# Kernel optimization log

Measured on AMD Instinct MI355X. Metric: run time of the kernel, lower is better.

The kernel has to match this reference:

```python
import jax, jax.numpy as jnp
import numpy as np

WINDOW = 128
CAUSAL = True
LOOK_BACKWARD = 1
LOOK_FORWARD = 0  # causal forces look_forward = 0


def _look_around(x, backward, forward, pad_value, dim):
    # pad along window axis (axis=1), then concat shifted slices along `dim`
    nw = x.shape[1]
    pad_cfg = [(0, 0)] * x.ndim
    pad_cfg[1] = (backward, forward)
    padded = jnp.pad(x, pad_cfg, constant_values=pad_value)
    slices = [padded[:, i:i + nw] for i in range(forward + backward + 1)]
    return jnp.concatenate(slices, axis=dim)


def setup_inputs() -> dict:
    key = jax.random.key(0)
    kq, kk, kv = jax.random.split(key, 3)
    shape = (2, 16, 4096, 64)
    return {
        "q": jax.random.normal(kq, shape, dtype=jnp.float32),
        "k": jax.random.normal(kk, shape, dtype=jnp.float32),
        "v": jax.random.normal(kv, shape, dtype=jnp.float32),
    }


def reference(q, k, v):
    b, h, t, e = q.shape
    scale = e ** (-0.5)
    windows = t // WINDOW  # t assumed divisible by WINDOW (pad_to_multiple is no-op)

    # merge batch and heads, bucket into windows
    bq = q.reshape(b * h, windows, WINDOW, e)
    bk = k.reshape(b * h, windows, WINDOW, e)
    bv = v.reshape(b * h, windows, WINDOW, e)

    # look-around gather of key/value windows: j-dim = WINDOW*(1+back+fwd)
    bk = _look_around(bk, LOOK_BACKWARD, LOOK_FORWARD, 0.0, dim=2)
    bv = _look_around(bv, LOOK_BACKWARD, LOOK_FORWARD, 0.0, dim=2)

    # positional indices for masking
    bq_t = jnp.arange(t).reshape(1, windows, WINDOW)
    bq_k = _look_around(bq_t, LOOK_BACKWARD, LOOK_FORWARD, -1, dim=2)

    mask = (bq_k == -1)[:, :, None, :]  # (1, w, 1, j) padded positions
    if CAUSAL:
        mask = mask | (bq_t[:, :, :, None] < bq_k[:, :, None, :])

    dots = jnp.einsum('bwie,bwje->bwij', bq * scale, bk)
    mask_value = -jnp.finfo(dots.dtype).max
    dots = jnp.where(mask, mask_value, dots)
    attn = jax.nn.softmax(dots.astype(jnp.float32), axis=-1).astype(dots.dtype)
    out = jnp.einsum('bwij,bwje->bwie', attn, bv)
    return out.reshape(b, h, t, e)
```

## Files before the change

kernel.cpp:

```cpp
#include <hip/hip_runtime.h>

#define T_DIM 4096
#define E_DIM 64
#define WIN   128
#define NWIN  (T_DIM / WIN)
#define KS_LD 72
#define VT_LD 136
#define OS_LD 68

typedef __bf16  bf16x4 __attribute__((ext_vector_type(4)));
typedef __bf16  bf16x8 __attribute__((ext_vector_type(8)));
typedef float   f32x16 __attribute__((ext_vector_type(16)));

__global__ __launch_bounds__(256, 4)
void la_fwd(const float* __restrict__ Q, const float* __restrict__ K,
            const float* __restrict__ V, float* __restrict__ O)
{
  __shared__ __align__(16) unsigned char lds_raw[35840];
  __bf16* Ks = (__bf16*)(lds_raw);
  __bf16* Vt = (__bf16*)(lds_raw + 18432);
  float*  Os = (float*)(lds_raw);

  const int tid  = threadIdx.x;
  const int lane = tid & 63;
  const int wid  = tid >> 6;
  const int col  = lane & 31;
  const int half = lane >> 5;

  const int flat = blockIdx.x;
  const int w  = (flat >> 3) & 31;
  const int bh = (flat & 7) * 4 + (flat >> 8);

  const float* Qb = Q + (size_t)bh * T_DIM * E_DIM;
  const float* Kb = K + (size_t)bh * T_DIM * E_DIM;
  const float* Vb = V + (size_t)bh * T_DIM * E_DIM;
  float*       Ob = O + (size_t)bh * T_DIM * E_DIM;

  const int q0 = w * WIN;
  const int eg = tid & 15;
  const int j0 = (tid >> 4) * 8;

  const float* kp1 = Kb + (size_t)q0 * E_DIM;
  const float* vp1 = Vb + (size_t)q0 * E_DIM;
  const float* kp0 = kp1 - WIN * E_DIM;
  const float* vp0 = vp1 - WIN * E_DIM;

  auto stageK = [&](const float* kp) {
    float4 kf[8];
#pragma unroll
    for (int i = 0; i < 8; ++i) kf[i] = *(const float4*)(kp + (i << 10) + (tid << 2));
#pragma unroll
    for (int i = 0; i < 8; ++i) {
      const int fi = (i << 10) + (tid << 2);
      bf16x4 k4;
      k4[0]=(__bf16)kf[i].x; k4[1]=(__bf16)kf[i].y; k4[2]=(__bf16)kf[i].z; k4[3]=(__bf16)kf[i].w;
      *(bf16x4*)(&Ks[(fi >> 6) * KS_LD + (fi & 63)]) = k4;
    }
  };
  auto stageV = [&](const float* vp) {
    float4 vf[8];
#pragma unroll
    for (int r = 0; r < 8; ++r)
      vf[r] = *(const float4*)(vp + (size_t)(j0 + r) * E_DIM + eg * 4);
#pragma unroll
    for (int c = 0; c < 4; ++c) {
      bf16x8 t;
#pragma unroll
      for (int r = 0; r < 8; ++r) t[r] = (__bf16)(((const float*)&vf[r])[c]);
      *(bf16x8*)(&Vt[(eg * 4 + c) * VT_LD + j0]) = t;
    }
  };

  const float QS = 0.125f * 1.44269504088896340736f;
  float4 qf[8];
  {
    const float* qrow = Qb + (size_t)(q0 + wid * 32 + col) * E_DIM;
#pragma unroll
    for (int c = 0; c < 4; ++c) {
      qf[2 * c]     = *(const float4*)(qrow + c * 16 + half * 8);
      qf[2 * c + 1] = *(const float4*)(qrow + c * 16 + half * 8 + 4);
    }
  }
  if (w > 0) { stageK(kp0); stageV(vp0); }
  else       { stageK(kp1); stageV(vp1); }

  bf16x8 bq[4];
#pragma unroll
  for (int c = 0; c < 4; ++c) {
    const float* x = (const float*)&qf[2 * c];
    const float* y = (const float*)&qf[2 * c + 1];
    bf16x8 a;
    a[0]=(__bf16)(x[0]*QS); a[1]=(__bf16)(x[1]*QS); a[2]=(__bf16)(x[2]*QS); a[3]=(__bf16)(x[3]*QS);
    a[4]=(__bf16)(y[0]*QS); a[5]=(__bf16)(y[1]*QS); a[6]=(__bf16)(y[2]*QS); a[7]=(__bf16)(y[3]*QS);
    bq[c] = a;
  }

  float  lsum = 0.0f;
  f32x16 oacc[2];
#pragma unroll
  for (int et = 0; et < 2; ++et)
#pragma unroll
    for (int r = 0; r < 16; ++r) oacc[et][r] = 0.0f;

  __syncthreads();

  auto kb_step = [&](int kb, bool diag) {
    f32x16 s;
#pragma unroll
    for (int r = 0; r < 16; ++r) s[r] = 0.0f;
#pragma unroll
    for (int c = 0; c < 4; ++c) {
      const bf16x8 a = *(const bf16x8*)(&Ks[(kb * 32 + col) * KS_LD + c * 16 + half * 8]);
      s = __builtin_amdgcn_mfma_f32_32x32x16_bf16(a, bq[c], s, 0, 0, 0);
    }
    float pr[16];
#pragma unroll
    for (int r = 0; r < 16; ++r) {
      const int key = (r & 3) + 8 * (r >> 2) + 4 * half;
      float sv = s[r];
      if (diag && key > col) sv = -3.0e38f;
      const float p = __builtin_amdgcn_exp2f(sv);
      lsum += p;
      pr[r] = p;
    }
#pragma unroll
    for (int g = 0; g < 2; ++g) {
      int A0, A1, B0, B1;
      asm("v_cvt_pk_bf16_f32 %0, %1, %2" : "=v"(A0) : "v"(pr[8*g+0]), "v"(pr[8*g+1]));
      asm("v_cvt_pk_bf16_f32 %0, %1, %2" : "=v"(A1) : "v"(pr[8*g+2]), "v"(pr[8*g+3]));
      asm("v_cvt_pk_bf16_f32 %0, %1, %2" : "=v"(B0) : "v"(pr[8*g+4]), "v"(pr[8*g+5]));
      asm("v_cvt_pk_bf16_f32 %0, %1, %2" : "=v"(B1) : "v"(pr[8*g+6]), "v"(pr[8*g+7]));
      asm("v_permlane32_swap_b32 %0, %1" : "+v"(A0), "+v"(B0));
      asm("v_permlane32_swap_b32 %0, %1" : "+v"(A1), "+v"(B1));
      union { int d[4]; bf16x8 v; } u;
      u.d[0] = A0; u.d[1] = A1; u.d[2] = B0; u.d[3] = B1;
      const int j0v = kb * 32 + g * 16 + half * 8;
#pragma unroll
      for (int et = 0; et < 2; ++et) {
        const bf16x8 bv = *(const bf16x8*)(&Vt[(et * 32 + col) * VT_LD + j0v]);
        oacc[et] = __builtin_amdgcn_mfma_f32_32x32x16_bf16(u.v, bv, oacc[et], 0, 0, 0);
      }
    }
  };

  if (w > 0) {
#pragma unroll
    for (int kb = 0; kb < 4; ++kb) kb_step(kb, false);
    __syncthreads();
    stageK(kp1);
    stageV(vp1);
    __syncthreads();
  }
#pragma unroll
  for (int kb = 0; kb < 4; ++kb)
    if (kb <= wid) kb_step(kb, kb == wid);

  float xx = lsum, yy = lsum;
  asm("v_permlane32_swap_b32 %0, %1" : "+v"(xx), "+v"(yy));
  const float ltot = xx + yy;

  __syncthreads();
#pragma unroll
  for (int r = 0; r < 16; ++r) {
    const int row = (r & 3) + 8 * (r >> 2) + 4 * half;
    const float lq   = __int_as_float(__builtin_amdgcn_ds_bpermute(row << 2, __float_as_int(ltot)));
    const float rinv = __builtin_amdgcn_rcpf(lq);
    Os[(wid * 32 + row) * OS_LD + col]      = oacc[0][r] * rinv;
    Os[(wid * 32 + row) * OS_LD + col + 32] = oacc[1][r] * rinv;
  }
  __syncthreads();
  {
    float* ob = Ob + (size_t)q0 * E_DIM;
#pragma unroll
    for (int i = 0; i < 8; ++i) {
      const int fi = (i << 10) + (tid << 2);
      const float4 o4 = *(const float4*)(&Os[(fi >> 6) * OS_LD + (fi & 63)]);
      *(float4*)(ob + fi) = o4;
    }
  }
}

extern "C" void kernel_launch(void* const* d_in, const int* in_sizes, int n_in,
                              void* d_out, int out_size, void* d_ws, size_t ws_size,
                              hipStream_t stream) {
  const float* Q = (const float*)d_in[0];
  const float* K = (const float*)d_in[1];
  const float* V = (const float*)d_in[2];
  float*       O = (float*)d_out;
  const int bh = in_sizes[0] / (T_DIM * E_DIM);
  la_fwd<<<dim3(NWIN * bh), 256, 0, stream>>>(Q, K, V, O);
}
```

Measured before the change: 140.8 us.

## Prefetch current K/V window into registers and swizzle LDS layouts

Issues global loads for both the previous and current K/V windows up front, holding the current window converted to bf16 in registers so its latency overlaps the first window's compute. LDS padding is replaced with XOR swizzles for K and transposed V, which shrinks shared memory to 32KB. The block index mapping also changes from a custom flattened remap to a plain 2D grid. The trade-off is higher register pressure from holding the prefetched tiles, and the output staging buffer loses its padding, which may cause bank conflicts.

```diff
diff --git a/kernel.cpp b/kernel.cpp
--- a/kernel.cpp
+++ b/kernel.cpp
@@ -4,9 +4,8 @@
 #define E_DIM 64
 #define WIN   128
 #define NWIN  (T_DIM / WIN)
-#define KS_LD 72
-#define VT_LD 136
-#define OS_LD 68
+#define K_B   16384
+#define V_B   16384
 
 typedef __bf16  bf16x4 __attribute__((ext_vector_type(4)));
 typedef __bf16  bf16x8 __attribute__((ext_vector_type(8)));
@@ -16,10 +15,10 @@
 void la_fwd(const float* __restrict__ Q, const float* __restrict__ K,
             const float* __restrict__ V, float* __restrict__ O)
 {
-  __shared__ __align__(16) unsigned char lds_raw[35840];
-  __bf16* Ks = (__bf16*)(lds_raw);
-  __bf16* Vt = (__bf16*)(lds_raw + 18432);
-  float*  Os = (float*)(lds_raw);
+  __shared__ __align__(16) unsigned char lds_raw[K_B + V_B];
+  unsigned char* KsB = lds_raw;
+  unsigned char* VtB = lds_raw + K_B;
+  float*         Os  = (float*)lds_raw;
 
   const int tid  = threadIdx.x;
   const int lane = tid & 63;
@@ -27,72 +26,105 @@
   const int col  = lane & 31;
   const int half = lane >> 5;
 
-  const int flat = blockIdx.x;
-  const int w  = (flat >> 3) & 31;
-  const int bh = (flat & 7) * 4 + (flat >> 8);
+  const int w  = blockIdx.x;
+  const int bh = blockIdx.y;
 
   const float* Qb = Q + (size_t)bh * T_DIM * E_DIM;
   const float* Kb = K + (size_t)bh * T_DIM * E_DIM;
   const float* Vb = V + (size_t)bh * T_DIM * E_DIM;
   float*       Ob = O + (size_t)bh * T_DIM * E_DIM;
 
-  const int q0 = w * WIN;
-  const int eg = tid & 15;
-  const int j0 = (tid >> 4) * 8;
-
-  const float* kp1 = Kb + (size_t)q0 * E_DIM;
-  const float* vp1 = Vb + (size_t)q0 * E_DIM;
-  const float* kp0 = kp1 - WIN * E_DIM;
-  const float* vp0 = vp1 - WIN * E_DIM;
-
-  auto stageK = [&](const float* kp) {
-    float4 kf[8];
-#pragma unroll
-    for (int i = 0; i < 8; ++i) kf[i] = *(const float4*)(kp + (i << 10) + (tid << 2));
+  const int q0  = w * WIN;
+  const int eg  = tid & 15;
+  const int j0v = (tid >> 4) * 8;
+
+  auto ldK = [&](int kr0, float4* f) {
+    const float* p = Kb + (size_t)kr0 * E_DIM;
+#pragma unroll
+    for (int i = 0; i < 8; ++i) f[i] = *(const float4*)(p + (i << 10) + (tid << 2));
+  };
+  auto ldV = [&](int kr0, float4* f) {
+    const float* p = Vb + (size_t)kr0 * E_DIM;
+#pragma unroll
+    for (int r = 0; r < 8; ++r)
+      f[r] = *(const float4*)(p + (size_t)(j0v + r) * E_DIM + eg * 4);
+  };
+  auto cvtK = [&](const float4* f, bf16x4* b) {
 #pragma unroll
     for (int i = 0; i < 8; ++i) {
-      const int fi = (i << 10) + (tid << 2);
       bf16x4 k4;
-      k4[0]=(__bf16)kf[i].x; k4[1]=(__bf16)kf[i].y; k4[2]=(__bf16)kf[i].z; k4[3]=(__bf16)kf[i].w;
-      *(bf16x4*)(&Ks[(fi >> 6) * KS_LD + (fi & 63)]) = k4;
-    }
-  };
-  auto stageV = [&](const float* vp) {
-    float4 vf[8];
-#pragma unroll
-    for (int r = 0; r < 8; ++r)
-      vf[r] = *(const float4*)(vp + (size_t)(j0 + r) * E_DIM + eg * 4);
-#pragma unroll
-    for (int c = 0; c < 4; ++c) {
-      bf16x8 t;
-#pragma unroll
-      for (int r = 0; r < 8; ++r) t[r] = (__bf16)(((const float*)&vf[r])[c]);
-      *(bf16x8*)(&Vt[(eg * 4 + c) * VT_LD + j0]) = t;
-    }
-  };
-
+      k4[0]=(__bf16)f[i].x; k4[1]=(__bf16)f[i].y; k4[2]=(__bf16)f[i].z; k4[3]=(__bf16)f[i].w;
+      b[i] = k4;
+    }
+  };
+  auto trV = [&](const float4* f, bf16x8* t) {
+#pragma unroll
+    for (int c = 0; c < 4; ++c) {
+      bf16x8 v8;
+#pragma unroll
+      for (int r = 0; r < 8; ++r) v8[r] = (__bf16)(((const float*)&f[r])[c]);
+      t[c] = v8;
+    }
+  };
+  auto wrK = [&](const bf16x4* b) {
+#pragma unroll
+    for (int i = 0; i < 8; ++i) {
+      const int fi  = (i << 10) + (tid << 2);
+      const int key = fi >> 6, e0 = fi & 63;
+      *(bf16x4*)(KsB + key * 128 + ((2 * e0) ^ ((key & 7) << 4))) = b[i];
+    }
+  };
+  auto wrV = [&](const bf16x8* t) {
+#pragma unroll
+    for (int c = 0; c < 4; ++c) {
+      const int e   = eg * 4 + c;
+      const int sig = ((e >> 2) & 3) | (((e ^ (e >> 4)) & 1) << 2);
+      *(bf16x8*)(VtB + e * 256 + ((2 * j0v) ^ (sig << 4))) = t[c];
+    }
+  };
   const float QS = 0.125f * 1.44269504088896340736f;
-  float4 qf[8];
-  {
+  auto ldQmk = [&](bf16x8* bq) {
+    float4 qf[8];
     const float* qrow = Qb + (size_t)(q0 + wid * 32 + col) * E_DIM;
 #pragma unroll
     for (int c = 0; c < 4; ++c) {
       qf[2 * c]     = *(const float4*)(qrow + c * 16 + half * 8);
       qf[2 * c + 1] = *(const float4*)(qrow + c * 16 + half * 8 + 4);
     }
-  }
-  if (w > 0) { stageK(kp0); stageV(vp0); }
-  else       { stageK(kp1); stageV(vp1); }
+#pragma unroll
+    for (int c = 0; c < 4; ++c) {
+      const float* x = (const float*)&qf[2 * c];
+      const float* y = (const float*)&qf[2 * c + 1];
+      bf16x8 a;
+      a[0]=(__bf16)(x[0]*QS); a[1]=(__bf16)(x[1]*QS); a[2]=(__bf16)(x[2]*QS); a[3]=(__bf16)(x[3]*QS);
+      a[4]=(__bf16)(y[0]*QS); a[5]=(__bf16)(y[1]*QS); a[6]=(__bf16)(y[2]*QS); a[7]=(__bf16)(y[3]*QS);
+      bq[c] = a;
+    }
+  };
 
   bf16x8 bq[4];
-#pragma unroll
-  for (int c = 0; c < 4; ++c) {
-    const float* x = (const float*)&qf[2 * c];
-    const float* y = (const float*)&qf[2 * c + 1];
-    bf16x8 a;
-    a[0]=(__bf16)(x[0]*QS); a[1]=(__bf16)(x[1]*QS); a[2]=(__bf16)(x[2]*QS); a[3]=(__bf16)(x[3]*QS);
-    a[4]=(__bf16)(y[0]*QS); a[5]=(__bf16)(y[1]*QS); a[6]=(__bf16)(y[2]*QS); a[7]=(__bf16)(y[3]*QS);
-    bq[c] = a;
+  bf16x4 kCur[8];
+  bf16x8 vCur[4];
+
+  if (w > 0) {
+    {
+      float4 kf[8], vf[8];
+      ldK(q0 - WIN, kf); ldV(q0 - WIN, vf);
+      ldQmk(bq);
+      bf16x4 kb_[8]; cvtK(kf, kb_); wrK(kb_);
+      bf16x8 vb_[4]; trV(vf, vb_);  wrV(vb_);
+    }
+    {
+      float4 kf[8], vf[8];
+      ldK(q0, kf); ldV(q0, vf);
+      cvtK(kf, kCur); trV(vf, vCur);
+    }
+  } else {
+    float4 kf[8], vf[8];
+    ldK(q0, kf); ldV(q0, vf);
+    ldQmk(bq);
+    bf16x4 kb_[8]; cvtK(kf, kb_); wrK(kb_);
+    bf16x8 vb_[4]; trV(vf, vb_);  wrV(vb_);
   }
 
   float  lsum = 0.0f;
@@ -110,7 +142,9 @@
     for (int r = 0; r < 16; ++r) s[r] = 0.0f;
 #pragma unroll
     for (int c = 0; c < 4; ++c) {
-      const bf16x8 a = *(const bf16x8*)(&Ks[(kb * 32 + col) * KS_LD + c * 16 + half * 8]);
+      const int key = kb * 32 + col;
+      const bf16x8 a = *(const bf16x8*)(KsB + key * 128 +
+                                        ((c * 32 + half * 16) ^ ((key & 7) << 4)));
       s = __builtin_amdgcn_mfma_f32_32x32x16_bf16(a, bq[c], s, 0, 0, 0);
     }
     float pr[16];
@@ -134,10 +168,12 @@
       asm("v_permlane32_swap_b32 %0, %1" : "+v"(A1), "+v"(B1));
       union { int d[4]; bf16x8 v; } u;
       u.d[0] = A0; u.d[1] = A1; u.d[2] = B0; u.d[3] = B1;
-      const int j0v = kb * 32 + g * 16 + half * 8;
+      const int jb = kb * 64 + g * 32 + half * 16;
 #pragma unroll
       for (int et = 0; et < 2; ++et) {
-        const bf16x8 bv = *(const bf16x8*)(&Vt[(et * 32 + col) * VT_LD + j0v]);
+        const int e   = et * 32 + col;
+        const int sig = ((e >> 2) & 3) | (((e ^ (e >> 4)) & 1) << 2);
+        const bf16x8 bv = *(const bf16x8*)(VtB + e * 256 + (jb ^ (sig << 4)));
         oacc[et] = __builtin_amdgcn_mfma_f32_32x32x16_bf16(u.v, bv, oacc[et], 0, 0, 0);
       }
     }
@@ -147,8 +183,7 @@
 #pragma unroll
     for (int kb = 0; kb < 4; ++kb) kb_step(kb, false);
     __syncthreads();
-    stageK(kp1);
-    stageV(vp1);
+    wrK(kCur); wrV(vCur);
     __syncthreads();
   }
 #pragma unroll
@@ -165,8 +200,8 @@
     const int row = (r & 3) + 8 * (r >> 2) + 4 * half;
     const float lq   = __int_as_float(__builtin_amdgcn_ds_bpermute(row << 2, __float_as_int(ltot)));
     const float rinv = __builtin_amdgcn_rcpf(lq);
-    Os[(wid * 32 + row) * OS_LD + col]      = oacc[0][r] * rinv;
-    Os[(wid * 32 + row) * OS_LD + col + 32] = oacc[1][r] * rinv;
+    Os[(wid * 32 + row) * 64 + col]      = oacc[0][r] * rinv;
+    Os[(wid * 32 + row) * 64 + col + 32] = oacc[1][r] * rinv;
   }
   __syncthreads();
   {
@@ -174,7 +209,7 @@
 #pragma unroll
     for (int i = 0; i < 8; ++i) {
       const int fi = (i << 10) + (tid << 2);
-      const float4 o4 = *(const float4*)(&Os[(fi >> 6) * OS_LD + (fi & 63)]);
+      const float4 o4 = *(const float4*)(&Os[fi]);
       *(float4*)(ob + fi) = o4;
     }
   }
@@ -188,5 +223,5 @@
   const float* V = (const float*)d_in[2];
   float*       O = (float*)d_out;
   const int bh = in_sizes[0] / (T_DIM * E_DIM);
-  la_fwd<<<dim3(NWIN * bh), 256, 0, stream>>>(Q, K, V, O);
+  la_fwd<<<dim3(NWIN, bh), 256, 0, stream>>>(Q, K, V, O);
 }
```

Result: slower. 144.5 us (+2.6%).
